# Optimization experiments

Hardware: AMD Instinct MI355X
Metric: run time of the kernel (lower is better)

Reference implementation:

```python
import jax, jax.numpy as jnp
import numpy as np

N = 8192
IN_DIM = 256
HID = 256
OUT_DIM = 256
P_DIM = 3
SIGMA = 1.0


def setup_inputs() -> dict:
    key = jax.random.key(0)
    ks = jax.random.split(key, 7)
    s_in = 1.0 / np.sqrt(IN_DIM)
    inp = {
        "X": jax.random.normal(ks[0], (N, IN_DIM + P_DIM), dtype=jnp.float32),
        "WQ": jax.random.uniform(ks[1], (IN_DIM, HID), jnp.float32, -s_in, s_in),
        "bQ": jax.random.uniform(ks[2], (HID,), jnp.float32, -s_in, s_in),
        "WK": jax.random.uniform(ks[3], (IN_DIM, HID), jnp.float32, -s_in, s_in),
        "bK": jax.random.uniform(ks[4], (HID,), jnp.float32, -s_in, s_in),
        "WV": jax.random.uniform(ks[5], (IN_DIM, OUT_DIM), jnp.float32, -s_in, s_in),
        "bV": jax.random.uniform(ks[6], (OUT_DIM,), jnp.float32, -s_in, s_in),
    }
    return inp


def _softmax_one(x):
    # exp(x - max) / (1 + sum(exp(x - max))) -- faithful to the torch softmax_one
    m = jnp.max(x, axis=-1, keepdims=True)
    e = jnp.exp(x - m)
    return e / (1.0 + jnp.sum(e, axis=-1, keepdims=True))


def reference(X, WQ, bQ, WK, bK, WV, bV):
    P = X[:, -P_DIM:]            # [N, 3] spatial coords
    Xf = X[:, :-P_DIM]           # [N, IN_DIM] features

    Q = Xf @ WQ + bQ             # [N, HID]
    K = Xf @ WK + bK             # [N, HID]
    V = Xf @ WV + bV             # [N, OUT_DIM]

    scores = (Q @ K.T) / jnp.sqrt(jnp.asarray(HID, Xf.dtype))  # [N, N]

    # squared pairwise distances ||P_i - P_j||^2 (cdist(P,P)**2)
    sq = jnp.sum(P * P, axis=-1)                                # [N]
    d2 = jnp.maximum(sq[:, None] + sq[None, :] - 2.0 * (P @ P.T), 0.0)
    decay = jnp.exp(-d2 / (2.0 * SIGMA ** 2))                   # [N, N]

    A = _softmax_one(scores * decay)                             # [N, N]
    H = A @ V                                                    # [N, OUT_DIM]
    # residual: input_dim == output_dim so res_proj is None
    return H + Xf
```

## Files before the change

kernel.cpp:

```cpp
#include <hip/hip_runtime.h>
#include <hip/hip_bf16.h>
#include <stdint.h>

#define NTOK 8192
#define XSTRIDE 259
#define LOG2E 1.4426950408889634f
#define DECC (-3.4712336270551023f)
#define KSPLIT 8
#define SPLEN (NTOK / KSPLIT)
#define BN 64
#define ITERS (SPLEN / BN)

typedef __bf16 bf16x8 __attribute__((ext_vector_type(8)));
typedef float f32x4 __attribute__((ext_vector_type(4)));
typedef float f32x16 __attribute__((ext_vector_type(16)));
typedef unsigned short u16;

union BF8 { u16 u[8]; bf16x8 v; };
union PW  { uint32_t u[4]; bf16x8 v; };

__device__ __forceinline__ u16 f2bf(float f) {
  uint32_t u = __float_as_uint(f);
  u += 0x7FFFu + ((u >> 16) & 1u);
  return (u16)(u >> 16);
}
__device__ __forceinline__ float bf2f(u16 h) {
  return __uint_as_float(((uint32_t)h) << 16);
}
__device__ __forceinline__ float exp2_hw(float x) {
  float r; asm("v_exp_f32 %0, %1" : "=v"(r) : "v"(x)); return r;
}
__device__ __forceinline__ f32x4 mfma16(bf16x8 a, bf16x8 b, f32x4 c) {
  return __builtin_amdgcn_mfma_f32_16x16x32_bf16(a, b, c, 0, 0, 0);
}
__device__ __forceinline__ f32x16 mfma32(bf16x8 a, bf16x8 b, f32x16 c) {
  return __builtin_amdgcn_mfma_f32_32x32x16_bf16(a, b, c, 0, 0, 0);
}
__device__ __forceinline__ void async16(const void* g, void* l) {
  __builtin_amdgcn_global_load_lds(
      (const __attribute__((address_space(1))) uint32_t*)g,
      (__attribute__((address_space(3))) uint32_t*)l, 16, 0, 0);
}
__device__ __forceinline__ void bsplit(float v, u16& h, u16& l) {
  h = f2bf(v);
  l = f2bf(v - bf2f(h));
}

__global__ __launch_bounds__(256) void xb_kernel(
    const float* __restrict__ X, u16* __restrict__ Xb,
    u16* __restrict__ Qp, u16* __restrict__ Kp) {
  const int t = threadIdx.x;
  const int row = blockIdx.x * 8 + (t >> 5);
  const int c0 = (t & 31) * 8;
  const float* xp = X + (size_t)row * XSTRIDE + c0;
  union { u16 u[8]; uint4 v; } o;
#pragma unroll
  for (int j = 0; j < 8; ++j) o.u[j] = f2bf(xp[j]);
  *(uint4*)(Xb + (size_t)row * 256 + c0) = o.v;

  if (t < 8) {
    const int r = blockIdx.x * 8 + t;
    const float* pp = X + (size_t)r * XSTRIDE + 256;
    const float x = pp[0], y = pp[1], z = pp[2];
    const float w = 0.5f * (x * x + y * y + z * z);
    u16 xh, xl, yh, yl, zh, zl, wh, wl;
    bsplit(x, xh, xl); bsplit(y, yh, yl); bsplit(z, zh, zl); bsplit(w, wh, wl);
    const u16 one = 0x3F80u;
    const u16 SGN = 0x8000u;
    union { u16 u[16]; uint4 v4[2]; } uq, uk;
    uq.u[0] = wh;  uk.u[0] = one;
    uq.u[1] = wl;  uk.u[1] = one;
    uq.u[2] = one; uk.u[2] = wh;
    uq.u[3] = one; uk.u[3] = wl;
    uq.u[4] = (u16)(xh ^ SGN); uk.u[4] = xh;
    uq.u[5] = (u16)(xh ^ SGN); uk.u[5] = xl;
    uq.u[6] = (u16)(xl ^ SGN); uk.u[6] = xh;
    uq.u[7] = (u16)(yh ^ SGN); uk.u[7] = yh;
    uq.u[8] = (u16)(yh ^ SGN); uk.u[8] = yl;
    uq.u[9] = (u16)(yl ^ SGN); uk.u[9] = yh;
    uq.u[10] = (u16)(zh ^ SGN); uk.u[10] = zh;
    uq.u[11] = (u16)(zh ^ SGN); uk.u[11] = zl;
    uq.u[12] = (u16)(zl ^ SGN); uk.u[12] = zh;
    uq.u[13] = 0; uk.u[13] = 0;
    uq.u[14] = 0; uk.u[14] = 0;
    uq.u[15] = 0; uk.u[15] = 0;
    ((uint4*)Qp)[r * 2] = uq.v4[0];
    ((uint4*)Qp)[r * 2 + 1] = uq.v4[1];
    ((uint4*)Kp)[r * 2] = uk.v4[0];
    ((uint4*)Kp)[r * 2 + 1] = uk.v4[1];
  }
}

__global__ __launch_bounds__(256) void wprep_kernel(
    const float* __restrict__ WQ, const float* __restrict__ WK,
    const float* __restrict__ WV, u16* __restrict__ Wt) {
  const int o = blockIdx.x;
  const int which = o >> 8, oo = o & 255;
  const float* W = (which == 0) ? WQ : ((which == 1) ? WK : WV);
  const int k = threadIdx.x;
  Wt[(size_t)o * 256 + k] = f2bf(W[(size_t)k * 256 + oo]);
}

__global__ __launch_bounds__(256) void qkv_kernel(
    const u16* __restrict__ Xb, const u16* __restrict__ Wt,
    const float* __restrict__ bQ, const float* __restrict__ bK,
    const float* __restrict__ bV,
    u16* __restrict__ Qb, u16* __restrict__ Kb, u16* __restrict__ Vt) {
  __shared__ u16 smem[64 * 256];
  const int tid = threadIdx.x;
  const int lane = tid & 63;
  const int wave = tid >> 6;
  const int l15 = lane & 15;
  const int q4 = lane >> 4;
  const int rb = blockIdx.x;
  const int ch = blockIdx.y;
  const int which = ch >> 2;
  const int c0 = (ch & 3) * 64;
  const float* bias = (which == 0) ? bQ : ((which == 1) ? bK : bV);

  bf16x8 xa[2][8];
#pragma unroll
  for (int mt = 0; mt < 2; ++mt) {
    const int row = rb * 128 + wave * 32 + mt * 16 + l15;
#pragma unroll
    for (int kc = 0; kc < 8; ++kc)
      xa[mt][kc] = *(const bf16x8*)(Xb + (size_t)row * 256 + kc * 32 + q4 * 8);
  }
  {
    const u16* Wsrc = Wt + (size_t)(which * 256 + c0) * 256;
    const int rb0 = wave * 16;
#pragma unroll
    for (int i = 0; i < 8; ++i) {
      int r = rb0 + i * 2 + (lane >> 5);
      int c = (lane & 31) ^ (r & 7);
      async16(Wsrc + (size_t)r * 256 + c * 8, smem + (rb0 + i * 2) * 256);
    }
  }
  asm volatile("s_waitcnt vmcnt(0)" ::: "memory");
  __syncthreads();

  f32x4 acc[2][4];
#pragma unroll
  for (int mt = 0; mt < 2; ++mt)
#pragma unroll
    for (int nt = 0; nt < 4; ++nt) acc[mt][nt] = (f32x4){0.f, 0.f, 0.f, 0.f};

#pragma unroll
  for (int kc = 0; kc < 8; ++kc) {
#pragma unroll
    for (int nt = 0; nt < 4; ++nt) {
      bf16x8 wf = *(const bf16x8*)(smem + (nt * 16 + l15) * 256 +
                                   (((kc * 4 + q4) ^ (l15 & 7)) * 8));
#pragma unroll
      for (int mt = 0; mt < 2; ++mt)
        acc[mt][nt] = mfma16(xa[mt][kc], wf, acc[mt][nt]);
    }
  }
  float bc[4];
#pragma unroll
  for (int nt = 0; nt < 4; ++nt) bc[nt] = bias[c0 + nt * 16 + l15];

  __syncthreads();
  const int grow0 = rb * 128;

  if (which == 2) {
#pragma unroll
    for (int mt = 0; mt < 2; ++mt)
#pragma unroll
      for (int nt = 0; nt < 4; ++nt) {
        const int lcol = nt * 16 + l15;
        const int lrow0 = wave * 32 + mt * 16 + q4 * 4;
        union { u16 u[4]; uint2 w; } p;
#pragma unroll
        for (int r = 0; r < 4; ++r) p.u[r] = f2bf(acc[mt][nt][r] + bc[nt]);
        *(uint2*)(smem + lcol * 136 + lrow0) = p.w;
      }
    __syncthreads();
#pragma unroll
    for (int i = 0; i < 4; ++i) {
      int chn = i * 256 + tid;
      int lcol = chn >> 4, s = chn & 15;
      uint4 d = *(const uint4*)(smem + lcol * 136 + s * 8);
      *(uint4*)(Vt + (size_t)(c0 + lcol) * NTOK + grow0 + s * 8) = d;
    }
  } else {
#pragma unroll
    for (int mt = 0; mt < 2; ++mt)
#pragma unroll
      for (int nt = 0; nt < 4; ++nt)
#pragma unroll
        for (int r = 0; r < 4; ++r)
          smem[(wave * 32 + mt * 16 + q4 * 4 + r) * 72 + nt * 16 + l15] =
              f2bf(acc[mt][nt][r] + bc[nt]);
    __syncthreads();
#pragma unroll
    for (int i = 0; i < 4; ++i) {
      int chn = i * 256 + tid;
      int lrow = chn >> 3, g = chn & 7;
      uint4 d = *(const uint4*)(smem + lrow * 72 + g * 8);
      int grow = grow0 + lrow, gc = c0 + g * 8;
      if (which == 1)
        *(uint4*)(Kb + (size_t)grow * 256 + gc) = d;
      else
        *(uint4*)(Qb + (size_t)((grow >> 5) * 16 + (gc >> 4)) * 512 +
                  ((gc >> 3) & 1) * 256 + (grow & 31) * 8) = d;
    }
  }
}

__global__ __launch_bounds__(512, 2) void attn_kernel(
    const u16* __restrict__ Qb, const u16* __restrict__ Kb,
    const u16* __restrict__ Vt, const u16* __restrict__ Qp,
    const u16* __restrict__ Kp, u16* __restrict__ Op,
    float* __restrict__ ml) {
  __shared__ u16 kbuf[2][BN * 256];
  __shared__ u16 vbuf[2][256 * BN];
  __shared__ u16 kpbuf[2][BN * 16];

  const int tid = threadIdx.x;
  const int lane = tid & 63;
  const int wave = tid >> 6;
  const int l31 = lane & 31;
  const int h5 = lane >> 5;
  const int sp = blockIdx.x;
  const int rb = blockIdx.y;
  const int q0 = rb * 256;
  const int wrow = wave * 32;

#define STAGE(T, S_)                                                          \
  do {                                                                        \
    const int key0_ = sp * SPLEN + (T) * BN;                                  \
    _Pragma("unroll")                                                         \
    for (int j = 0; j < 4; ++j) {                                             \
      int r = wave * 8 + j * 2 + (lane >> 5);                                 \
      int c = (lane & 31) ^ (r & 7);                                          \
      async16(Kb + (size_t)(key0_ + r) * 256 + c * 8,                         \
              &kbuf[S_][(wave * 8 + j * 2) * 256]);                           \
    }                                                                         \
    _Pragma("unroll")                                                         \
    for (int j = 0; j < 4; ++j) {                                             \
      int f = wave * 32 + j * 8 + (lane >> 3);                                \
      int c = (lane & 7) ^ (f & 7);                                           \
      async16(Vt + (size_t)f * NTOK + key0_ + c * 8,                          \
              &vbuf[S_][(wave * 32 + j * 8) * BN]);                           \
    }                                                                         \
    if (wave == 0) {                                                          \
      _Pragma("unroll")                                                       \
      for (int hh = 0; hh < 2; ++hh)                                          \
        async16(Kp + (size_t)(key0_ + hh * 32 + (lane >> 1)) * 16 +           \
                    (lane & 1) * 8,                                           \
                &kpbuf[S_][hh * 32 * 16]);                                    \
    }                                                                         \
  } while (0)

  const int rb32 = rb * 8 + wave;
  bf16x8 qa[16];
#pragma unroll
  for (int kc = 0; kc < 16; ++kc)
    qa[kc] = *(const bf16x8*)(Qb + ((size_t)(rb32 * 16 + kc) * 64 + lane) * 8);

  const bf16x8 qp = *(const bf16x8*)(Qp + (size_t)(q0 + wrow + l31) * 16 +
                                     h5 * 8);

  f32x16 O[8];
#pragma unroll
  for (int ft = 0; ft < 8; ++ft)
#pragma unroll
    for (int r = 0; r < 16; ++r) O[ft][r] = 0.f;
  float lrow = 0.f;

  const int swz = l31 & 7;

  STAGE(0, 0);

#pragma unroll 1
  for (int t = 0; t < ITERS; ++t) {
    const int slot = t & 1;
    asm volatile("s_waitcnt vmcnt(0)" ::: "memory");
    __builtin_amdgcn_s_barrier();
    if (t + 1 < ITERS) STAGE(t + 1, slot ^ 1);

#pragma unroll
    for (int sub = 0; sub < 2; ++sub) {
      f32x16 T;
#pragma unroll
      for (int r = 0; r < 16; ++r) T[r] = 0.f;
      {
        bf16x8 kpf = *(const bf16x8*)(&kpbuf[slot][(sub * 32 + l31) * 16 +
                                      h5 * 8]);
        T = mfma32(kpf, qp, T);
      }

      f32x16 S;
#pragma unroll
      for (int r = 0; r < 16; ++r) S[r] = 0.f;
      __builtin_amdgcn_s_setprio(1);
#pragma unroll
      for (int kc = 0; kc < 16; ++kc) {
        bf16x8 kf = *(const bf16x8*)(&kbuf[slot][(sub * 32 + l31) * 256 +
                                     (((2 * kc + h5) ^ swz) * 8)]);
        S = mfma32(kf, qa[kc], S);
      }
      __builtin_amdgcn_s_setprio(0);

#pragma unroll
      for (int r = 0; r < 16; ++r) {
        float dec = exp2_hw(fmaf(T[r], -LOG2E, DECC));
        float p = exp2_hw(S[r] * dec);
        S[r] = p;
        lrow += p;
      }

      uint32_t w0, w1, w2, w3, w4, w5, w6, w7;
      asm("v_cvt_pk_bf16_f32 %0, %1, %2" : "=v"(w0) : "v"(S[0]),  "v"(S[1]));
      asm("v_cvt_pk_bf16_f32 %0, %1, %2" : "=v"(w1) : "v"(S[2]),  "v"(S[3]));
      asm("v_cvt_pk_bf16_f32 %0, %1, %2" : "=v"(w2) : "v"(S[4]),  "v"(S[5]));
      asm("v_cvt_pk_bf16_f32 %0, %1, %2" : "=v"(w3) : "v"(S[6]),  "v"(S[7]));
      asm("v_cvt_pk_bf16_f32 %0, %1, %2" : "=v"(w4) : "v"(S[8]),  "v"(S[9]));
      asm("v_cvt_pk_bf16_f32 %0, %1, %2" : "=v"(w5) : "v"(S[10]), "v"(S[11]));
      asm("v_cvt_pk_bf16_f32 %0, %1, %2" : "=v"(w6) : "v"(S[12]), "v"(S[13]));
      asm("v_cvt_pk_bf16_f32 %0, %1, %2" : "=v"(w7) : "v"(S[14]), "v"(S[15]));
      asm volatile("v_permlane32_swap_b32 %0, %1" : "+v"(w2), "+v"(w0));
      asm volatile("v_permlane32_swap_b32 %0, %1" : "+v"(w3), "+v"(w1));
      asm volatile("v_permlane32_swap_b32 %0, %1" : "+v"(w6), "+v"(w4));
      asm volatile("v_permlane32_swap_b32 %0, %1" : "+v"(w7), "+v"(w5));
      PW pa0, pa1;
      pa0.u[0] = w0; pa0.u[1] = w1; pa0.u[2] = w2; pa0.u[3] = w3;
      pa1.u[0] = w4; pa1.u[1] = w5; pa1.u[2] = w6; pa1.u[3] = w7;

      __builtin_amdgcn_s_setprio(1);
#pragma unroll
      for (int kh = 0; kh < 2; ++kh) {
        const bf16x8 pa = kh ? pa1.v : pa0.v;
        const int khh = sub * 2 + kh;
#pragma unroll
        for (int ft = 0; ft < 8; ++ft) {
          bf16x8 vf = *(const bf16x8*)(&vbuf[slot][(ft * 32 + l31) * BN +
                                       (((2 * khh + h5) ^ swz) * 8)]);
          O[ft] = mfma32(pa, vf, O[ft]);
        }
      }
      __builtin_amdgcn_s_setprio(0);
    }
  }

  float lsum = lrow + __shfl_xor(lrow, 32);
#pragma unroll
  for (int ft = 0; ft < 8; ++ft)
#pragma unroll
    for (int r = 0; r < 16; ++r) {
      int row = q0 + wrow + (r & 3) + 8 * (r >> 2) + 4 * h5;
      Op[((size_t)sp * NTOK + row) * 256 + ft * 32 + l31] = f2bf(O[ft][r]);
    }
  if (lane < 32)
    ml[sp * NTOK + q0 + wrow + lane] = lsum;
#undef STAGE
}

__global__ __launch_bounds__(256) void combine_kernel(
    const float* __restrict__ X, const u16* __restrict__ Op,
    const float* __restrict__ ml, float* __restrict__ out) {
  const int row = blockIdx.x * 2 + (threadIdx.x >> 7);
  const int f2 = threadIdx.x & 127;
  float den = 1.f, n0 = 0.f, n1 = 0.f;
#pragma unroll
  for (int s = 0; s < KSPLIT; ++s) {
    den += ml[s * NTOK + row];
    uint32_t v = *(const uint32_t*)(Op + ((size_t)s * NTOK + row) * 256 +
                                    f2 * 2);
    n0 += bf2f((u16)v);
    n1 += bf2f((u16)(v >> 16));
  }
  const float inv = 1.f / den;
  float2 o;
  o.x = n0 * inv + X[(size_t)row * XSTRIDE + f2 * 2];
  o.y = n1 * inv + X[(size_t)row * XSTRIDE + f2 * 2 + 1];
  *(float2*)(out + (size_t)row * 256 + f2 * 2) = o;
}

extern "C" void kernel_launch(void* const* d_in, const int* in_sizes, int n_in,
                              void* d_out, int out_size, void* d_ws, size_t ws_size,
                              hipStream_t stream) {
  (void)in_sizes; (void)n_in; (void)out_size; (void)ws_size;
  const float* X  = (const float*)d_in[0];
  const float* WQ = (const float*)d_in[1];
  const float* bQ = (const float*)d_in[2];
  const float* WK = (const float*)d_in[3];
  const float* bK = (const float*)d_in[4];
  const float* WV = (const float*)d_in[5];
  const float* bV = (const float*)d_in[6];
  float* out = (float*)d_out;
  char* ws = (char*)d_ws;

  u16*   Qb = (u16*)(ws);
  u16*   Kb = (u16*)(ws + ((size_t)4 << 20));
  u16*   Vt = (u16*)(ws + ((size_t)8 << 20));
  u16*   Qp = (u16*)(ws + ((size_t)12 << 20));
  u16*   Kp = (u16*)(ws + ((size_t)12 << 20) + 262144);
  u16*   Wt = (u16*)(ws + ((size_t)12 << 20) + 524288);
  u16*   Xb = (u16*)(ws + ((size_t)12 << 20) + 524288 + 393216);
  float* ml = (float*)(ws + ((size_t)16 << 20) + 524288 + 393216);
  u16*   Op = (u16*)(ws + ((size_t)16 << 20) + 524288 + 393216 + 524288);

  xb_kernel<<<dim3(NTOK / 8), dim3(256), 0, stream>>>(X, Xb, Qp, Kp);
  wprep_kernel<<<dim3(768), dim3(256), 0, stream>>>(WQ, WK, WV, Wt);
  qkv_kernel<<<dim3(64, 12), dim3(256), 0, stream>>>(Xb, Wt, bQ, bK, bV,
                                                     Qb, Kb, Vt);
  attn_kernel<<<dim3(KSPLIT, NTOK / 256), dim3(512), 0, stream>>>(
      Qb, Kb, Vt, Qp, Kp, Op, ml);
  combine_kernel<<<dim3(NTOK / 2), dim3(256), 0, stream>>>(X, Op, ml, out);
}
```

Baseline: 205.7 us.

## Merge prep kernels and restructure QKV projection with double-buffered weight chunks

Folds the X-to-bf16 conversion and weight transpose into one prep kernel, removing a launch. The weight transpose now goes through an LDS tile so global reads and writes are coalesced, instead of strided per-element stores. The QKV kernel now uses 64-row blocks that loop over four 64-column weight chunks, double-buffering the async weight loads so X fragments are loaded once per block. The trade-off is more barriers per block and fewer total blocks.

Measured after the change: 200.7 us. 2.5% less time.

```diff
diff --git a/kernel.cpp b/kernel.cpp
--- a/kernel.cpp
+++ b/kernel.cpp
@@ -46,59 +46,74 @@
   l = f2bf(v - bf2f(h));
 }
 
-__global__ __launch_bounds__(256) void xb_kernel(
-    const float* __restrict__ X, u16* __restrict__ Xb,
-    u16* __restrict__ Qp, u16* __restrict__ Kp) {
+__global__ __launch_bounds__(256) void prep_kernel(
+    const float* __restrict__ X, const float* __restrict__ WQ,
+    const float* __restrict__ WK, const float* __restrict__ WV,
+    u16* __restrict__ Xb, u16* __restrict__ Qp, u16* __restrict__ Kp,
+    u16* __restrict__ Wt) {
+  const int bid = blockIdx.x;
   const int t = threadIdx.x;
-  const int row = blockIdx.x * 8 + (t >> 5);
-  const int c0 = (t & 31) * 8;
-  const float* xp = X + (size_t)row * XSTRIDE + c0;
-  union { u16 u[8]; uint4 v; } o;
-#pragma unroll
-  for (int j = 0; j < 8; ++j) o.u[j] = f2bf(xp[j]);
-  *(uint4*)(Xb + (size_t)row * 256 + c0) = o.v;
-
-  if (t < 8) {
-    const int r = blockIdx.x * 8 + t;
-    const float* pp = X + (size_t)r * XSTRIDE + 256;
-    const float x = pp[0], y = pp[1], z = pp[2];
-    const float w = 0.5f * (x * x + y * y + z * z);
-    u16 xh, xl, yh, yl, zh, zl, wh, wl;
-    bsplit(x, xh, xl); bsplit(y, yh, yl); bsplit(z, zh, zl); bsplit(w, wh, wl);
-    const u16 one = 0x3F80u;
-    const u16 SGN = 0x8000u;
-    union { u16 u[16]; uint4 v4[2]; } uq, uk;
-    uq.u[0] = wh;  uk.u[0] = one;
-    uq.u[1] = wl;  uk.u[1] = one;
-    uq.u[2] = one; uk.u[2] = wh;
-    uq.u[3] = one; uk.u[3] = wl;
-    uq.u[4] = (u16)(xh ^ SGN); uk.u[4] = xh;
-    uq.u[5] = (u16)(xh ^ SGN); uk.u[5] = xl;
-    uq.u[6] = (u16)(xl ^ SGN); uk.u[6] = xh;
-    uq.u[7] = (u16)(yh ^ SGN); uk.u[7] = yh;
-    uq.u[8] = (u16)(yh ^ SGN); uk.u[8] = yl;
-    uq.u[9] = (u16)(yl ^ SGN); uk.u[9] = yh;
-    uq.u[10] = (u16)(zh ^ SGN); uk.u[10] = zh;
-    uq.u[11] = (u16)(zh ^ SGN); uk.u[11] = zl;
-    uq.u[12] = (u16)(zl ^ SGN); uk.u[12] = zh;
-    uq.u[13] = 0; uk.u[13] = 0;
-    uq.u[14] = 0; uk.u[14] = 0;
-    uq.u[15] = 0; uk.u[15] = 0;
-    ((uint4*)Qp)[r * 2] = uq.v4[0];
-    ((uint4*)Qp)[r * 2 + 1] = uq.v4[1];
-    ((uint4*)Kp)[r * 2] = uk.v4[0];
-    ((uint4*)Kp)[r * 2 + 1] = uk.v4[1];
+  if (bid < NTOK / 8) {
+    const int row = bid * 8 + (t >> 5);
+    const int c0 = (t & 31) * 8;
+    const float* xp = X + (size_t)row * XSTRIDE + c0;
+    union { u16 u[8]; uint4 v; } o;
+#pragma unroll
+    for (int j = 0; j < 8; ++j) o.u[j] = f2bf(xp[j]);
+    *(uint4*)(Xb + (size_t)row * 256 + c0) = o.v;
+
+    if (t < 8) {
+      const int r = bid * 8 + t;
+      const float* pp = X + (size_t)r * XSTRIDE + 256;
+      const float x = pp[0], y = pp[1], z = pp[2];
+      const float w = 0.5f * (x * x + y * y + z * z);
+      u16 xh, xl, yh, yl, zh, zl, wh, wl;
+      bsplit(x, xh, xl); bsplit(y, yh, yl); bsplit(z, zh, zl);
+      bsplit(w, wh, wl);
+      const u16 one = 0x3F80u;
+      const u16 SGN = 0x8000u;
+      union { u16 u[16]; uint4 v4[2]; } uq, uk;
+      uq.u[0] = wh;  uk.u[0] = one;
+      uq.u[1] = wl;  uk.u[1] = one;
+      uq.u[2] = one; uk.u[2] = wh;
+      uq.u[3] = one; uk.u[3] = wl;
+      uq.u[4] = (u16)(xh ^ SGN); uk.u[4] = xh;
+      uq.u[5] = (u16)(xh ^ SGN); uk.u[5] = xl;
+      uq.u[6] = (u16)(xl ^ SGN); uk.u[6] = xh;
+      uq.u[7] = (u16)(yh ^ SGN); uk.u[7] = yh;
+      uq.u[8] = (u16)(yh ^ SGN); uk.u[8] = yl;
+      uq.u[9] = (u16)(yl ^ SGN); uk.u[9] = yh;
+      uq.u[10] = (u16)(zh ^ SGN); uk.u[10] = zh;
+      uq.u[11] = (u16)(zh ^ SGN); uk.u[11] = zl;
+      uq.u[12] = (u16)(zl ^ SGN); uk.u[12] = zh;
+      uq.u[13] = 0; uk.u[13] = 0;
+      uq.u[14] = 0; uk.u[14] = 0;
+      uq.u[15] = 0; uk.u[15] = 0;
+      ((uint4*)Qp)[r * 2] = uq.v4[0];
+      ((uint4*)Qp)[r * 2 + 1] = uq.v4[1];
+      ((uint4*)Kp)[r * 2] = uk.v4[0];
+      ((uint4*)Kp)[r * 2 + 1] = uk.v4[1];
+    }
+  } else {
+    __shared__ u16 T[32 * 264];
+    const int b2 = bid - NTOK / 8;
+    const int which = b2 >> 3, ob = b2 & 7;
+    const float* W = (which == 0) ? WQ : ((which == 1) ? WK : WV);
+    const int kk = t >> 5, oo = t & 31;
+#pragma unroll
+    for (int kc = 0; kc < 32; ++kc) {
+      const int k = kc * 8 + kk;
+      T[oo * 264 + k] = f2bf(W[(size_t)k * 256 + ob * 32 + oo]);
+    }
+    __syncthreads();
+#pragma unroll
+    for (int i = 0; i < 4; ++i) {
+      int chn = i * 256 + t;
+      int o2 = chn >> 5, s = chn & 31;
+      uint4 d = *(const uint4*)(T + o2 * 264 + s * 8);
+      *(uint4*)(Wt + (size_t)(which * 256 + ob * 32 + o2) * 256 + s * 8) = d;
+    }
   }
-}
-
-__global__ __launch_bounds__(256) void wprep_kernel(
-    const float* __restrict__ WQ, const float* __restrict__ WK,
-    const float* __restrict__ WV, u16* __restrict__ Wt) {
-  const int o = blockIdx.x;
-  const int which = o >> 8, oo = o & 255;
-  const float* W = (which == 0) ? WQ : ((which == 1) ? WK : WV);
-  const int k = threadIdx.x;
-  Wt[(size_t)o * 256 + k] = f2bf(W[(size_t)k * 256 + oo]);
 }
 
 __global__ __launch_bounds__(256) void qkv_kernel(
@@ -106,106 +121,106 @@
     const float* __restrict__ bQ, const float* __restrict__ bK,
     const float* __restrict__ bV,
     u16* __restrict__ Qb, u16* __restrict__ Kb, u16* __restrict__ Vt) {
-  __shared__ u16 smem[64 * 256];
+  __shared__ u16 wt[2][64 * 256];
   const int tid = threadIdx.x;
   const int lane = tid & 63;
   const int wave = tid >> 6;
   const int l15 = lane & 15;
   const int q4 = lane >> 4;
   const int rb = blockIdx.x;
-  const int ch = blockIdx.y;
-  const int which = ch >> 2;
-  const int c0 = (ch & 3) * 64;
+  const int which = blockIdx.y;
   const float* bias = (which == 0) ? bQ : ((which == 1) ? bK : bV);
-
-  bf16x8 xa[2][8];
-#pragma unroll
-  for (int mt = 0; mt < 2; ++mt) {
-    const int row = rb * 128 + wave * 32 + mt * 16 + l15;
+  const int grow0 = rb * 64;
+
+  bf16x8 xa[8];
+  {
+    const int row = grow0 + wave * 16 + l15;
 #pragma unroll
     for (int kc = 0; kc < 8; ++kc)
-      xa[mt][kc] = *(const bf16x8*)(Xb + (size_t)row * 256 + kc * 32 + q4 * 8);
+      xa[kc] = *(const bf16x8*)(Xb + (size_t)row * 256 + kc * 32 + q4 * 8);
   }
-  {
-    const u16* Wsrc = Wt + (size_t)(which * 256 + c0) * 256;
-    const int rb0 = wave * 16;
-#pragma unroll
-    for (int i = 0; i < 8; ++i) {
-      int r = rb0 + i * 2 + (lane >> 5);
-      int c = (lane & 31) ^ (r & 7);
-      async16(Wsrc + (size_t)r * 256 + c * 8, smem + (rb0 + i * 2) * 256);
-    }
-  }
-  asm volatile("s_waitcnt vmcnt(0)" ::: "memory");
-  __syncthreads();
-
-  f32x4 acc[2][4];
-#pragma unroll
-  for (int mt = 0; mt < 2; ++mt)
-#pragma unroll
-    for (int nt = 0; nt < 4; ++nt) acc[mt][nt] = (f32x4){0.f, 0.f, 0.f, 0.f};
-
-#pragma unroll
-  for (int kc = 0; kc < 8; ++kc) {
-#pragma unroll
-    for (int nt = 0; nt < 4; ++nt) {
-      bf16x8 wf = *(const bf16x8*)(smem + (nt * 16 + l15) * 256 +
-                                   (((kc * 4 + q4) ^ (l15 & 7)) * 8));
-#pragma unroll
-      for (int mt = 0; mt < 2; ++mt)
-        acc[mt][nt] = mfma16(xa[mt][kc], wf, acc[mt][nt]);
-    }
-  }
-  float bc[4];
-#pragma unroll
-  for (int nt = 0; nt < 4; ++nt) bc[nt] = bias[c0 + nt * 16 + l15];
-
-  __syncthreads();
-  const int grow0 = rb * 128;
-
-  if (which == 2) {
-#pragma unroll
-    for (int mt = 0; mt < 2; ++mt)
+
+#define STAGEW(C_, B_)                                                        \
+  do {                                                                        \
+    const u16* Wsrc = Wt + (size_t)(which * 256 + (C_) * 64) * 256;           \
+    const int rb0 = wave * 16;                                                \
+    _Pragma("unroll")                                                         \
+    for (int i = 0; i < 8; ++i) {                                             \
+      int r = rb0 + i * 2 + (lane >> 5);                                      \
+      int cc = (lane & 31) ^ (r & 7);                                         \
+      async16(Wsrc + (size_t)r * 256 + cc * 8, &wt[B_][(rb0 + i * 2) * 256]); \
+    }                                                                         \
+  } while (0)
+
+  STAGEW(0, 0);
+
+#pragma unroll 1
+  for (int c = 0; c < 4; ++c) {
+    const int cur = c & 1;
+    const int c0 = c * 64;
+    asm volatile("s_waitcnt vmcnt(0)" ::: "memory");
+    __syncthreads();
+    if (c < 3) STAGEW(c + 1, cur ^ 1);
+
+    f32x4 acc[4];
+#pragma unroll
+    for (int nt = 0; nt < 4; ++nt) acc[nt] = (f32x4){0.f, 0.f, 0.f, 0.f};
+#pragma unroll
+    for (int kc = 0; kc < 8; ++kc) {
+#pragma unroll
+      for (int nt = 0; nt < 4; ++nt) {
+        bf16x8 wf = *(const bf16x8*)(&wt[cur][(nt * 16 + l15) * 256 +
+                                     (((kc * 4 + q4) ^ (l15 & 7)) * 8)]);
+        acc[nt] = mfma16(xa[kc], wf, acc[nt]);
+      }
+    }
+    float bc[4];
+#pragma unroll
+    for (int nt = 0; nt < 4; ++nt) bc[nt] = bias[c0 + nt * 16 + l15];
+
+    __syncthreads();
+    u16* smem = &wt[cur][0];
+
+    if (which == 2) {
 #pragma unroll
       for (int nt = 0; nt < 4; ++nt) {
         const int lcol = nt * 16 + l15;
-        const int lrow0 = wave * 32 + mt * 16 + q4 * 4;
         union { u16 u[4]; uint2 w; } p;
 #pragma unroll
-        for (int r = 0; r < 4; ++r) p.u[r] = f2bf(acc[mt][nt][r] + bc[nt]);
-        *(uint2*)(smem + lcol * 136 + lrow0) = p.w;
-      }
-    __syncthreads();
-#pragma unroll
-    for (int i = 0; i < 4; ++i) {
-      int chn = i * 256 + tid;
-      int lcol = chn >> 4, s = chn & 15;
-      uint4 d = *(const uint4*)(smem + lcol * 136 + s * 8);
-      *(uint4*)(Vt + (size_t)(c0 + lcol) * NTOK + grow0 + s * 8) = d;
-    }
-  } else {
-#pragma unroll
-    for (int mt = 0; mt < 2; ++mt)
+        for (int r = 0; r < 4; ++r) p.u[r] = f2bf(acc[nt][r] + bc[nt]);
+        *(uint2*)(smem + lcol * 72 + wave * 16 + q4 * 4) = p.w;
+      }
+      __syncthreads();
+#pragma unroll
+      for (int i = 0; i < 2; ++i) {
+        int chn = i * 256 + tid;
+        int lcol = chn >> 3, s = chn & 7;
+        uint4 d = *(const uint4*)(smem + lcol * 72 + s * 8);
+        *(uint4*)(Vt + (size_t)(c0 + lcol) * NTOK + grow0 + s * 8) = d;
+      }
+    } else {
 #pragma unroll
       for (int nt = 0; nt < 4; ++nt)
 #pragma unroll
         for (int r = 0; r < 4; ++r)
-          smem[(wave * 32 + mt * 16 + q4 * 4 + r) * 72 + nt * 16 + l15] =
-              f2bf(acc[mt][nt][r] + bc[nt]);
-    __syncthreads();
-#pragma unroll
-    for (int i = 0; i < 4; ++i) {
-      int chn = i * 256 + tid;
-      int lrow = chn >> 3, g = chn & 7;
-      uint4 d = *(const uint4*)(smem + lrow * 72 + g * 8);
-      int grow = grow0 + lrow, gc = c0 + g * 8;
-      if (which == 1)
-        *(uint4*)(Kb + (size_t)grow * 256 + gc) = d;
-      else
-        *(uint4*)(Qb + (size_t)((grow >> 5) * 16 + (gc >> 4)) * 512 +
-                  ((gc >> 3) & 1) * 256 + (grow & 31) * 8) = d;
+          smem[(wave * 16 + q4 * 4 + r) * 72 + nt * 16 + l15] =
+              f2bf(acc[nt][r] + bc[nt]);
+      __syncthreads();
+#pragma unroll
+      for (int i = 0; i < 2; ++i) {
+        int chn = i * 256 + tid;
+        int lrow = chn >> 3, g = chn & 7;
+        uint4 d = *(const uint4*)(smem + lrow * 72 + g * 8);
+        int grow = grow0 + lrow, gc = c0 + g * 8;
+        if (which == 1)
+          *(uint4*)(Kb + (size_t)grow * 256 + gc) = d;
+        else
+          *(uint4*)(Qb + (size_t)((grow >> 5) * 16 + (gc >> 4)) * 512 +
+                    ((gc >> 3) & 1) * 256 + (grow & 31) * 8) = d;
+      }
     }
   }
+#undef STAGEW
 }
 
 __global__ __launch_bounds__(512, 2) void attn_kernel(
@@ -402,9 +417,9 @@
   float* ml = (float*)(ws + ((size_t)16 << 20) + 524288 + 393216);
   u16*   Op = (u16*)(ws + ((size_t)16 << 20) + 524288 + 393216 + 524288);
 
-  xb_kernel<<<dim3(NTOK / 8), dim3(256), 0, stream>>>(X, Xb, Qp, Kp);
-  wprep_kernel<<<dim3(768), dim3(256), 0, stream>>>(WQ, WK, WV, Wt);
-  qkv_kernel<<<dim3(64, 12), dim3(256), 0, stream>>>(Xb, Wt, bQ, bK, bV,
+  prep_kernel<<<dim3(NTOK / 8 + 24), dim3(256), 0, stream>>>(
+      X, WQ, WK, WV, Xb, Qp, Kp, Wt);
+  qkv_kernel<<<dim3(128, 3), dim3(256), 0, stream>>>(Xb, Wt, bQ, bK, bV,
                                                      Qb, Kb, Vt);
   attn_kernel<<<dim3(KSPLIT, NTOK / 256), dim3(512), 0, stream>>>(
       Qb, Kb, Vt, Qp, Kp, Op, ml);
```
